# Performance work log

Hardware: AMD Instinct MI355X
Metric: run time of the kernel (lower is better)

The kernel has to match this reference:

```python
import jax, jax.numpy as jnp
import numpy as np
from jax import lax

B, T, I, H, L, C = 128, 784, 1, 256, 20, 10  # batch, seq_len, input, hidden, layers, classes


def setup_inputs() -> dict:
    key = jax.random.key(0)
    ks = jax.random.split(key, 9)
    s = 1.0 / np.sqrt(H)  # torch nn.RNN init: U(-1/sqrt(H), 1/sqrt(H))
    u = lambda k, shape: jax.random.uniform(k, shape, jnp.float32, -s, s)
    return {
        "x": jax.random.normal(ks[0], (B, T, I), jnp.float32),
        "W_ih0": u(ks[1], (H, I)),        # layer 0 input proj
        "b_ih0": u(ks[2], (H,)),
        "W_ih": u(ks[3], (L - 1, H, H)),  # layers 1..L-1 input proj
        "b_ih": u(ks[4], (L - 1, H)),
        "W_hh": u(ks[5], (L, H, H)),      # recurrent weights, all layers
        "b_hh": u(ks[6], (L, H)),
        "W_fc": u(ks[7], (C, H)),         # classification head
        "b_fc": u(ks[8], (C,)),
    }


def _rnn_layer(x_seq, W_ih, b_ih, W_hh, b_hh):
    """One vanilla relu-RNN layer. x_seq: [B,T,in] -> [B,T,H]."""
    # Hoist the input projection out of the scan (batched GEMM over all timesteps).
    xp = jnp.einsum('bti,hi->bth', x_seq, W_ih) + b_ih  # [B,T,H]
    h0 = jnp.zeros((x_seq.shape[0], W_hh.shape[0]), x_seq.dtype)

    def step(h, xt):
        h = jax.nn.relu(xt + h @ W_hh.T + b_hh)
        return h, h

    _, ys = lax.scan(step, h0, jnp.swapaxes(xp, 0, 1))  # scan over time
    return jnp.swapaxes(ys, 0, 1)  # [B,T,H]


def reference(x, W_ih0, b_ih0, W_ih, b_ih, W_hh, b_hh, W_fc, b_fc):
    h = _rnn_layer(x, W_ih0, b_ih0, W_hh[0], b_hh[0])
    for l in range(L - 1):  # fixed small layer loop
        h = _rnn_layer(h, W_ih[l], b_ih[l], W_hh[l + 1], b_hh[l + 1])
    last_hidden = h[:, -1, :]  # [B,H]
    return last_hidden @ W_fc.T + b_fc  # [B,C]
```

## Files before the change

### kernel.cpp

```cpp
#include <hip/hip_runtime.h>
#include <hip/hip_fp16.h>


#define B_    128
#define T_    784
#define H_    256
#define L_    20
#define C_    10
#define G_    8
#define BM_   16
#define S_    4
#define NS_   196
#define SW_   280
#define XSW_  260
#define RQWS_ 4096
#define TPB_  512
#define HW_   4
#define NT_   4

typedef _Float16 v8h __attribute__((ext_vector_type(8)));
typedef _Float16 v4h __attribute__((ext_vector_type(4)));
typedef float    v4f __attribute__((ext_vector_type(4)));
typedef unsigned long long u64;

union U64H { u64 u; _Float16 h[4]; };

__device__ __forceinline__ void bar_lds() {
    asm volatile("s_waitcnt lgkmcnt(0)" ::: "memory");
    __builtin_amdgcn_s_barrier();
    asm volatile("" ::: "memory");
}
__device__ __forceinline__ void bar_full() {
    asm volatile("s_waitcnt vmcnt(0) lgkmcnt(0)" ::: "memory");
    __builtin_amdgcn_s_barrier();
    asm volatile("" ::: "memory");
}

__global__ __launch_bounds__(TPB_, 2)
void rnn_wavefront(const float* __restrict__ x,
                   const float* __restrict__ W_ih0,
                   const float* __restrict__ b_ih0,
                   const float* __restrict__ W_ih,
                   const float* __restrict__ b_ih,
                   const float* __restrict__ W_hh,
                   const float* __restrict__ b_hh,
                   const float* __restrict__ W_fc,
                   const float* __restrict__ b_fc,
                   float* __restrict__ out,
                   unsigned* __restrict__ prod,
                   unsigned* __restrict__ cons,
                   u64* __restrict__ ring,
                   int rmask)
{
    const int l    = blockIdx.x >> 3;
    const int g    = blockIdx.x & 7;
    const int tid  = threadIdx.x;
    const int lane = tid & 63;
    const int wave = tid >> 6;
    const bool hwv = wave < HW_;
    const int wsub = hwv ? wave : wave - HW_;
    const int quad = lane >> 4;
    const int s16  = lane & 15;
    const int nbase = wsub * 64;
    const int m_e  = tid >> 5;
    const int n_e  = (tid & 31) * 8;

    __shared__ __align__(16) _Float16 bufX[2][S_][BM_][SW_];
    __shared__ __align__(16) _Float16 lH[2][BM_][SW_];
    __shared__ __align__(16) _Float16 xps[2][S_][BM_][XSW_];

    for (int i = tid; i < 2 * BM_ * SW_; i += TPB_) (&lH[0][0][0])[i] = (_Float16)0.f;

    v8h wf[8][NT_];
#pragma unroll
    for (int kt = 0; kt < 8; ++kt) {
        const int k0 = kt * 32 + quad * 8;
#pragma unroll
        for (int nt = 0; nt < NT_; ++nt) {
            const int j = nbase + nt * 16 + s16;
            v8h w;
            if (hwv) {
                const float* src = &W_hh[(((size_t)l * H_) + j) * H_ + k0];
#pragma unroll
                for (int i = 0; i < 8; ++i) w[i] = (_Float16)src[i];
            } else if (l > 0) {
                const float* src = &W_ih[(((size_t)(l - 1) * H_) + j) * H_ + k0];
#pragma unroll
                for (int i = 0; i < 8; ++i) w[i] = (_Float16)src[i];
            } else {
#pragma unroll
                for (int i = 0; i < 8; ++i) w[i] = (_Float16)0.f;
            }
            wf[kt][nt] = w;
        }
    }

    float bias[NT_][4], w0v[NT_][4];
    if (!hwv) {
#pragma unroll
        for (int nt = 0; nt < NT_; ++nt)
#pragma unroll
            for (int r = 0; r < 4; ++r) {
                const int j = nbase + nt * 16 + quad * 4 + r;
                bias[nt][r] = b_hh[l * H_ + j] +
                              ((l == 0) ? b_ih0[j] : b_ih[(l - 1) * H_ + j]);
                w0v[nt][r]  = (l == 0) ? W_ih0[j] : 0.f;
            }
    }

    unsigned* upprod = prod + ((l > 0 ? l - 1 : 0) * G_ + g);
    unsigned* myprod = prod + (l * G_ + g);
    unsigned* mycons = cons + (l * G_ + g);
    unsigned* dncons = cons + (((l < L_ - 1) ? l + 1 : l) * G_ + g);
    const unsigned R = (unsigned)rmask + 1u;
    u64* myring = ring + ((size_t)(l * G_ + g) * (size_t)R) * RQWS_;
    u64* upring = ring + ((size_t)((l > 0 ? l - 1 : 0) * G_ + g) * (size_t)R) * RQWS_;

    unsigned pSeen = 0, cSeen = 0;
    const size_t eidx = (size_t)m_e * 64 + (size_t)(tid & 31) * 2;

    if (l > 0) {
        if (tid == 64) {
            while (pSeen < 2u) {
                pSeen = __hip_atomic_load(upprod, __ATOMIC_RELAXED,
                                          __HIP_MEMORY_SCOPE_AGENT);
                if (pSeen < 2u) __builtin_amdgcn_s_sleep(2);
            }
        }
        __syncthreads();
#pragma unroll
        for (int sl = 0; sl < 2; ++sl)
#pragma unroll
            for (int jj = 0; jj < S_; ++jj) {
                u64 v0 = __hip_atomic_load(upring + (size_t)sl * RQWS_ + (size_t)jj * 1024 + eidx,
                                           __ATOMIC_RELAXED, __HIP_MEMORY_SCOPE_AGENT);
                u64 v1 = __hip_atomic_load(upring + (size_t)sl * RQWS_ + (size_t)jj * 1024 + eidx + 1,
                                           __ATOMIC_RELAXED, __HIP_MEMORY_SCOPE_AGENT);
                *(u64*)&bufX[sl][jj][m_e][n_e]     = v0;
                *(u64*)&bufX[sl][jj][m_e][n_e + 4] = v1;
            }
        __syncthreads();
    }
    if (!hwv) {
#pragma unroll
        for (int jj = 0; jj < S_; ++jj) {
            v4f xpa[NT_];
#pragma unroll
            for (int nt = 0; nt < NT_; ++nt)
                xpa[nt] = (v4f){bias[nt][0], bias[nt][1], bias[nt][2], bias[nt][3]};
            if (l > 0) {
#pragma unroll
                for (int kt = 0; kt < 8; ++kt) {
                    v8h a = *(const v8h*)&bufX[0][jj][s16][kt * 32 + quad * 8];
#pragma unroll
                    for (int nt = 0; nt < NT_; ++nt)
                        xpa[nt] = __builtin_amdgcn_mfma_f32_16x16x32_f16(
                                      wf[kt][nt], a, xpa[nt], 0, 0, 0);
                }
            } else {
                const float xv = x[(size_t)(g * BM_ + s16) * T_ + jj];
#pragma unroll
                for (int nt = 0; nt < NT_; ++nt)
#pragma unroll
                    for (int r = 0; r < 4; ++r)
                        xpa[nt][r] = bias[nt][r] + xv * w0v[nt][r];
            }
#pragma unroll
            for (int nt = 0; nt < NT_; ++nt) {
                U64H pk;
#pragma unroll
                for (int r = 0; r < 4; ++r) pk.h[r] = (_Float16)xpa[nt][r];
                *(u64*)&xps[0][jj][s16][nbase + nt * 16 + quad * 4] = pk.u;
            }
        }
    }
    __syncthreads();

    for (int s = 0; s < NS_; ++s) {
        const bool stOK = (l > 0) && (s + 2 < NS_);
        const bool xOK  = (s + 1 < NS_);
        u64 pfv[S_][2];

#pragma unroll
        for (int j = 0; j < S_; ++j) {
            const int t = S_ * s + j;
            if (j == 1) bar_full(); else bar_lds();

            if (j == 0) {
                if (tid == 0 && l > 0) {
                    const unsigned cv = (unsigned)((s + 2 <= NS_) ? s + 2 : NS_);
                    __hip_atomic_store(mycons, cv, __ATOMIC_RELAXED,
                                       __HIP_MEMORY_SCOPE_AGENT);
                }
                if (tid == 64 && stOK) {
                    const unsigned tgt = (unsigned)(s + 3);
                    while (pSeen < tgt) {
                        pSeen = __hip_atomic_load(upprod, __ATOMIC_RELAXED,
                                                  __HIP_MEMORY_SCOPE_AGENT);
                        if (pSeen < tgt) __builtin_amdgcn_s_sleep(2);
                    }
                }
                if (tid == 128 && l < L_ - 1 && s >= (int)R) {
                    const unsigned tgt = (unsigned)(s - (int)R + 1);
                    while (cSeen < tgt) {
                        cSeen = __hip_atomic_load(dncons, __ATOMIC_RELAXED,
                                                  __HIP_MEMORY_SCOPE_AGENT);
                        if (cSeen < tgt) __builtin_amdgcn_s_sleep(2);
                    }
                }
            }

            if (j == 1) {
                if (tid == 0 && l < L_ - 1 && s >= 1)
                    __hip_atomic_store(myprod, (unsigned)s, __ATOMIC_RELAXED,
                                       __HIP_MEMORY_SCOPE_AGENT);
                if (stOK) {
                    const u64* base = upring + (size_t)((s + 2) & rmask) * RQWS_;
#pragma unroll
                    for (int jj = 0; jj < S_; ++jj) {
                        pfv[jj][0] = __hip_atomic_load(base + (size_t)jj * 1024 + eidx,
                                                       __ATOMIC_RELAXED,
                                                       __HIP_MEMORY_SCOPE_AGENT);
                        pfv[jj][1] = __hip_atomic_load(base + (size_t)jj * 1024 + eidx + 1,
                                                       __ATOMIC_RELAXED,
                                                       __HIP_MEMORY_SCOPE_AGENT);
                    }
                }
            }

            if (l < L_ - 1 && t > 0) {
                u64 e0 = *(const u64*)&lH[t & 1][m_e][n_e];
                u64 e1 = *(const u64*)&lH[t & 1][m_e][n_e + 4];
                u64* d = myring + (size_t)(((t - 1) >> 2) & rmask) * RQWS_
                                + (size_t)((t - 1) & 3) * 1024 + eidx;
                __hip_atomic_store(d,     e0, __ATOMIC_RELAXED, __HIP_MEMORY_SCOPE_AGENT);
                __hip_atomic_store(d + 1, e1, __ATOMIC_RELAXED, __HIP_MEMORY_SCOPE_AGENT);
            }

            if (hwv) {
                v4h xph[NT_];
#pragma unroll
                for (int nt = 0; nt < NT_; ++nt)
                    xph[nt] = *(const v4h*)&xps[s & 1][j][s16][nbase + nt * 16 + quad * 4];

                v4f acc[NT_];
#pragma unroll
                for (int nt = 0; nt < NT_; ++nt) acc[nt] = (v4f){0.f, 0.f, 0.f, 0.f};
#pragma unroll
                for (int kt = 0; kt < 8; ++kt) {
                    v8h a = *(const v8h*)&lH[t & 1][s16][kt * 32 + quad * 8];
#pragma unroll
                    for (int nt = 0; nt < NT_; ++nt)
                        acc[nt] = __builtin_amdgcn_mfma_f32_16x16x32_f16(
                                      wf[kt][nt], a, acc[nt], 0, 0, 0);
                }
#pragma unroll
                for (int nt = 0; nt < NT_; ++nt) {
                    U64H pk;
#pragma unroll
                    for (int r = 0; r < 4; ++r) {
                        float v = (float)xph[nt][r] + acc[nt][r];
                        v = fmaxf(v, 0.f);
                        pk.h[r] = (_Float16)v;
                    }
                    *(u64*)&lH[(t + 1) & 1][s16][nbase + nt * 16 + quad * 4] = pk.u;
                }
            } else if (xOK) {
                v4f xpa[NT_];
#pragma unroll
                for (int nt = 0; nt < NT_; ++nt)
                    xpa[nt] = (v4f){bias[nt][0], bias[nt][1], bias[nt][2], bias[nt][3]};
                if (l > 0) {
#pragma unroll
                    for (int kt = 0; kt < 8; ++kt) {
                        v8h a = *(const v8h*)&bufX[(s + 1) & 1][j][s16][kt * 32 + quad * 8];
#pragma unroll
                        for (int nt = 0; nt < NT_; ++nt)
                            xpa[nt] = __builtin_amdgcn_mfma_f32_16x16x32_f16(
                                          wf[kt][nt], a, xpa[nt], 0, 0, 0);
                    }
                } else {
                    const float xv = x[(size_t)(g * BM_ + s16) * T_ + (S_ * (s + 1) + j)];
#pragma unroll
                    for (int nt = 0; nt < NT_; ++nt)
#pragma unroll
                        for (int r = 0; r < 4; ++r)
                            xpa[nt][r] = bias[nt][r] + xv * w0v[nt][r];
                }
#pragma unroll
                for (int nt = 0; nt < NT_; ++nt) {
                    U64H pk;
#pragma unroll
                    for (int r = 0; r < 4; ++r) pk.h[r] = (_Float16)xpa[nt][r];
                    *(u64*)&xps[(s + 1) & 1][j][s16][nbase + nt * 16 + quad * 4] = pk.u;
                }
            }

            if (j == S_ - 1 && stOK) {
#pragma unroll
                for (int jj = 0; jj < S_; ++jj) {
                    *(u64*)&bufX[s & 1][jj][m_e][n_e]     = pfv[jj][0];
                    *(u64*)&bufX[s & 1][jj][m_e][n_e + 4] = pfv[jj][1];
                }
            }
        }
    }

    if (l < L_ - 1) {
        u64 e0 = *(const u64*)&lH[0][m_e][n_e];
        u64 e1 = *(const u64*)&lH[0][m_e][n_e + 4];
        u64* d = myring + (size_t)(((T_ - 1) >> 2) & rmask) * RQWS_
                        + (size_t)3 * 1024 + eidx;
        __hip_atomic_store(d,     e0, __ATOMIC_RELAXED, __HIP_MEMORY_SCOPE_AGENT);
        __hip_atomic_store(d + 1, e1, __ATOMIC_RELAXED, __HIP_MEMORY_SCOPE_AGENT);
        __syncthreads();
        if (tid == 0)
            __hip_atomic_store(myprod, (unsigned)NS_, __ATOMIC_RELAXED,
                               __HIP_MEMORY_SCOPE_AGENT);
    } else {
        __syncthreads();
        if (tid < BM_ * C_) {
            const int bl = tid / C_;
            const int c  = tid % C_;
            float sum = b_fc[c];
            for (int k = 0; k < H_; ++k) sum += (float)lH[0][bl][k] * W_fc[c * H_ + k];
            out[(size_t)(g * BM_ + bl) * C_ + c] = sum;
        }
    }
}

extern "C" void kernel_launch(void* const* d_in, const int* in_sizes, int n_in,
                              void* d_out, int out_size, void* d_ws, size_t ws_size,
                              hipStream_t stream) {
    const float* x     = (const float*)d_in[0];
    const float* W_ih0 = (const float*)d_in[1];
    const float* b_ih0 = (const float*)d_in[2];
    const float* W_ih  = (const float*)d_in[3];
    const float* b_ih  = (const float*)d_in[4];
    const float* W_hh  = (const float*)d_in[5];
    const float* b_hh  = (const float*)d_in[6];
    const float* W_fc  = (const float*)d_in[7];
    const float* b_fc  = (const float*)d_in[8];
    float* out = (float*)d_out;

    const size_t cntBytes = (size_t)L_ * G_ * sizeof(unsigned);
    unsigned* prod = (unsigned*)d_ws;
    unsigned* cons = (unsigned*)((char*)d_ws + cntBytes);
    u64* ring      = (u64*)((char*)d_ws + 2 * cntBytes);

    const size_t slotBytes = (size_t)RQWS_ * 8;
    const size_t base = 2 * cntBytes;
    int R = 4;
    if (ws_size >= base + (size_t)L_ * G_ * 16 * slotBytes) R = 16;
    else if (ws_size >= base + (size_t)L_ * G_ * 8 * slotBytes) R = 8;

    hipMemsetAsync(d_ws, 0, 2 * cntBytes, stream);

    rnn_wavefront<<<dim3(L_ * G_), dim3(TPB_), 0, stream>>>(
        x, W_ih0, b_ih0, W_ih, b_ih, W_hh, b_hh, W_fc, b_fc,
        out, prod, cons, ring, R - 1);
}
```

Measured before the change: 1.127 ms.

## Offload ring I/O to non-recurrent waves and prioritize recurrent waves

Moves all ring-buffer loads, stores and flag polling off the four recurrent-MFMA waves onto the four input-projection waves. Each of those threads now handles 16 halves instead of 8. The recurrent waves get raised scheduling priority via s_setprio, and they preload the whole group's xps projections once per 4-step group instead of once per step. The aim is to take global-memory latency and spin polling off the serial recurrence critical path. In exchange it raises register pressure and puts more I/O work on the projection waves.

```diff
diff --git a/kernel.cpp b/kernel.cpp
--- a/kernel.cpp
+++ b/kernel.cpp
@@ -62,8 +62,12 @@
     const int quad = lane >> 4;
     const int s16  = lane & 15;
     const int nbase = wsub * 64;
-    const int m_e  = tid >> 5;
-    const int n_e  = (tid & 31) * 8;
+
+    const int xtid = tid & 255;
+    const int m_e  = xtid >> 4;
+    const int c_e  = xtid & 15;
+    const int n_e  = c_e * 16;
+    const size_t eidx = (size_t)m_e * 64 + (size_t)c_e * 4;
 
     __shared__ __align__(16) _Float16 bufX[2][S_][BM_][SW_];
     __shared__ __align__(16) _Float16 lH[2][BM_][SW_];
@@ -117,10 +121,11 @@
     u64* upring = ring + ((size_t)((l > 0 ? l - 1 : 0) * G_ + g) * (size_t)R) * RQWS_;
 
     unsigned pSeen = 0, cSeen = 0;
-    const size_t eidx = (size_t)m_e * 64 + (size_t)(tid & 31) * 2;
+
+    if (hwv) __builtin_amdgcn_s_setprio(1);
 
     if (l > 0) {
-        if (tid == 64) {
+        if (tid == 256) {
             while (pSeen < 2u) {
                 pSeen = __hip_atomic_load(upprod, __ATOMIC_RELAXED,
                                           __HIP_MEMORY_SCOPE_AGENT);
@@ -128,17 +133,19 @@
             }
         }
         __syncthreads();
-#pragma unroll
-        for (int sl = 0; sl < 2; ++sl)
-#pragma unroll
-            for (int jj = 0; jj < S_; ++jj) {
-                u64 v0 = __hip_atomic_load(upring + (size_t)sl * RQWS_ + (size_t)jj * 1024 + eidx,
-                                           __ATOMIC_RELAXED, __HIP_MEMORY_SCOPE_AGENT);
-                u64 v1 = __hip_atomic_load(upring + (size_t)sl * RQWS_ + (size_t)jj * 1024 + eidx + 1,
-                                           __ATOMIC_RELAXED, __HIP_MEMORY_SCOPE_AGENT);
-                *(u64*)&bufX[sl][jj][m_e][n_e]     = v0;
-                *(u64*)&bufX[sl][jj][m_e][n_e + 4] = v1;
-            }
+        if (!hwv) {
+#pragma unroll
+            for (int sl = 0; sl < 2; ++sl)
+#pragma unroll
+                for (int jj = 0; jj < S_; ++jj)
+#pragma unroll
+                    for (int k = 0; k < 4; ++k) {
+                        u64 v = __hip_atomic_load(
+                            upring + (size_t)sl * RQWS_ + (size_t)jj * 1024 + eidx + k,
+                            __ATOMIC_RELAXED, __HIP_MEMORY_SCOPE_AGENT);
+                        *(u64*)&bufX[sl][jj][m_e][n_e + 4 * k] = v;
+                    }
+        }
         __syncthreads();
     }
     if (!hwv) {
@@ -179,7 +186,8 @@
     for (int s = 0; s < NS_; ++s) {
         const bool stOK = (l > 0) && (s + 2 < NS_);
         const bool xOK  = (s + 1 < NS_);
-        u64 pfv[S_][2];
+        u64 pfv[S_][4];
+        v4h xphv[S_][NT_];
 
 #pragma unroll
         for (int j = 0; j < S_; ++j) {
@@ -187,12 +195,12 @@
             if (j == 1) bar_full(); else bar_lds();
 
             if (j == 0) {
-                if (tid == 0 && l > 0) {
+                if (tid == 448 && l > 0) {
                     const unsigned cv = (unsigned)((s + 2 <= NS_) ? s + 2 : NS_);
                     __hip_atomic_store(mycons, cv, __ATOMIC_RELAXED,
                                        __HIP_MEMORY_SCOPE_AGENT);
                 }
-                if (tid == 64 && stOK) {
+                if (tid == 256 && stOK) {
                     const unsigned tgt = (unsigned)(s + 3);
                     while (pSeen < tgt) {
                         pSeen = __hip_atomic_load(upprod, __ATOMIC_RELAXED,
@@ -200,7 +208,7 @@
                         if (pSeen < tgt) __builtin_amdgcn_s_sleep(2);
                     }
                 }
-                if (tid == 128 && l < L_ - 1 && s >= (int)R) {
+                if (tid == 320 && l < L_ - 1 && s >= (int)R) {
                     const unsigned tgt = (unsigned)(s - (int)R + 1);
                     while (cSeen < tgt) {
                         cSeen = __hip_atomic_load(dncons, __ATOMIC_RELAXED,
@@ -208,41 +216,47 @@
                         if (cSeen < tgt) __builtin_amdgcn_s_sleep(2);
                     }
                 }
+                if (hwv) {
+#pragma unroll
+                    for (int jj = 0; jj < S_; ++jj)
+#pragma unroll
+                        for (int nt = 0; nt < NT_; ++nt)
+                            xphv[jj][nt] = *(const v4h*)
+                                &xps[s & 1][jj][s16][nbase + nt * 16 + quad * 4];
+                }
             }
 
             if (j == 1) {
-                if (tid == 0 && l < L_ - 1 && s >= 1)
+                if (tid == 448 && l < L_ - 1 && s >= 1)
                     __hip_atomic_store(myprod, (unsigned)s, __ATOMIC_RELAXED,
                                        __HIP_MEMORY_SCOPE_AGENT);
-                if (stOK) {
+                if (stOK && !hwv) {
                     const u64* base = upring + (size_t)((s + 2) & rmask) * RQWS_;
 #pragma unroll
-                    for (int jj = 0; jj < S_; ++jj) {
-                        pfv[jj][0] = __hip_atomic_load(base + (size_t)jj * 1024 + eidx,
-                                                       __ATOMIC_RELAXED,
-                                                       __HIP_MEMORY_SCOPE_AGENT);
-                        pfv[jj][1] = __hip_atomic_load(base + (size_t)jj * 1024 + eidx + 1,
-                                                       __ATOMIC_RELAXED,
-                                                       __HIP_MEMORY_SCOPE_AGENT);
-                    }
-                }
-            }
-
-            if (l < L_ - 1 && t > 0) {
-                u64 e0 = *(const u64*)&lH[t & 1][m_e][n_e];
-                u64 e1 = *(const u64*)&lH[t & 1][m_e][n_e + 4];
+                    for (int jj = 0; jj < S_; ++jj)
+#pragma unroll
+                        for (int k = 0; k < 4; ++k)
+                            pfv[jj][k] = __hip_atomic_load(
+                                base + (size_t)jj * 1024 + eidx + k,
+                                __ATOMIC_RELAXED, __HIP_MEMORY_SCOPE_AGENT);
+                }
+            }
+
+            if (!hwv && l < L_ - 1 && t > 0) {
+                u64 e[4];
+                e[0] = *(const u64*)&lH[t & 1][m_e][n_e];
+                e[1] = *(const u64*)&lH[t & 1][m_e][n_e + 4];
+                e[2] = *(const u64*)&lH[t & 1][m_e][n_e + 8];
+                e[3] = *(const u64*)&lH[t & 1][m_e][n_e + 12];
                 u64* d = myring + (size_t)(((t - 1) >> 2) & rmask) * RQWS_
                                 + (size_t)((t - 1) & 3) * 1024 + eidx;
-                __hip_atomic_store(d,     e0, __ATOMIC_RELAXED, __HIP_MEMORY_SCOPE_AGENT);
-                __hip_atomic_store(d + 1, e1, __ATOMIC_RELAXED, __HIP_MEMORY_SCOPE_AGENT);
+#pragma unroll
+                for (int k = 0; k < 4; ++k)
+                    __hip_atomic_store(d + k, e[k], __ATOMIC_RELAXED,
+                                       __HIP_MEMORY_SCOPE_AGENT);
             }
 
             if (hwv) {
-                v4h xph[NT_];
-#pragma unroll
-                for (int nt = 0; nt < NT_; ++nt)
-                    xph[nt] = *(const v4h*)&xps[s & 1][j][s16][nbase + nt * 16 + quad * 4];
-
                 v4f acc[NT_];
 #pragma unroll
                 for (int nt = 0; nt < NT_; ++nt) acc[nt] = (v4f){0.f, 0.f, 0.f, 0.f};
@@ -259,7 +273,7 @@
                     U64H pk;
 #pragma unroll
                     for (int r = 0; r < 4; ++r) {
-                        float v = (float)xph[nt][r] + acc[nt][r];
+                        float v = (float)xphv[j][nt][r] + acc[nt][r];
                         v = fmaxf(v, 0.f);
                         pk.h[r] = (_Float16)v;
                     }
@@ -296,25 +310,29 @@
                 }
             }
 
-            if (j == S_ - 1 && stOK) {
-#pragma unroll
-                for (int jj = 0; jj < S_; ++jj) {
-                    *(u64*)&bufX[s & 1][jj][m_e][n_e]     = pfv[jj][0];
-                    *(u64*)&bufX[s & 1][jj][m_e][n_e + 4] = pfv[jj][1];
-                }
+            if (j == S_ - 1 && stOK && !hwv) {
+#pragma unroll
+                for (int jj = 0; jj < S_; ++jj)
+#pragma unroll
+                    for (int k = 0; k < 4; ++k)
+                        *(u64*)&bufX[s & 1][jj][m_e][n_e + 4 * k] = pfv[jj][k];
             }
         }
     }
 
     if (l < L_ - 1) {
-        u64 e0 = *(const u64*)&lH[0][m_e][n_e];
-        u64 e1 = *(const u64*)&lH[0][m_e][n_e + 4];
-        u64* d = myring + (size_t)(((T_ - 1) >> 2) & rmask) * RQWS_
-                        + (size_t)3 * 1024 + eidx;
-        __hip_atomic_store(d,     e0, __ATOMIC_RELAXED, __HIP_MEMORY_SCOPE_AGENT);
-        __hip_atomic_store(d + 1, e1, __ATOMIC_RELAXED, __HIP_MEMORY_SCOPE_AGENT);
+        if (!hwv) {
+            u64* d = myring + (size_t)(((T_ - 1) >> 2) & rmask) * RQWS_
+                            + (size_t)3 * 1024 + eidx;
+#pragma unroll
+            for (int k = 0; k < 4; ++k) {
+                u64 e = *(const u64*)&lH[0][m_e][n_e + 4 * k];
+                __hip_atomic_store(d + k, e, __ATOMIC_RELAXED,
+                                   __HIP_MEMORY_SCOPE_AGENT);
+            }
+        }
         __syncthreads();
-        if (tid == 0)
+        if (tid == 448)
             __hip_atomic_store(myprod, (unsigned)NS_, __ATOMIC_RELAXED,
                                __HIP_MEMORY_SCOPE_AGENT);
     } else {
```

Measured after the change: 1.617 ms. +43.5%, slower.

## Decouple recurrent and projection waves with LDS flag handshakes instead of block barriers

Applied to the files above, without the earlier changes.

Drops the block-wide barrier per timestep and lets the four recurrent waves and four projection/IO waves run as separate producer/consumer roles, synchronised through LDS counter flags. The hidden-state buffer grows to eight slots so the recurrent waves can run ahead while the other waves publish finished steps to the ring and stage the next input slot in halves. The aim is to take ring I/O and input projection off the recurrence's critical path. The cost is busy-spinning on LDS flags that competes for issue slots, plus more complex ordering that relies on relaxed atomics and explicit waitcnts.

```diff
diff --git a/kernel.cpp b/kernel.cpp
--- a/kernel.cpp
+++ b/kernel.cpp
@@ -11,11 +11,10 @@
 #define BM_   16
 #define S_    4
 #define NS_   196
-#define SW_   280
+#define SW_   264
 #define XSW_  260
 #define RQWS_ 4096
 #define TPB_  512
-#define HW_   4
 #define NT_   4
 
 typedef _Float16 v8h __attribute__((ext_vector_type(8)));
@@ -25,15 +24,47 @@
 
 union U64H { u64 u; _Float16 h[4]; };
 
-__device__ __forceinline__ void bar_lds() {
-    asm volatile("s_waitcnt lgkmcnt(0)" ::: "memory");
-    __builtin_amdgcn_s_barrier();
-    asm volatile("" ::: "memory");
-}
-__device__ __forceinline__ void bar_full() {
-    asm volatile("s_waitcnt vmcnt(0) lgkmcnt(0)" ::: "memory");
-    __builtin_amdgcn_s_barrier();
-    asm volatile("" ::: "memory");
+__device__ __forceinline__ void lgkm0() { asm volatile("s_waitcnt lgkmcnt(0)" ::: "memory"); }
+__device__ __forceinline__ void vm0()   { asm volatile("s_waitcnt vmcnt(0)"   ::: "memory"); }
+__device__ __forceinline__ void cbar()  { asm volatile("" ::: "memory"); }
+
+__device__ __forceinline__ void flagst(unsigned* p, unsigned v) {
+    cbar();
+    __hip_atomic_store(p, v, __ATOMIC_RELAXED, __HIP_MEMORY_SCOPE_WORKGROUP);
+}
+__device__ __forceinline__ void spin4(const unsigned* f, unsigned tgt) {
+    const volatile u64* p = (const volatile u64*)f;
+    for (;;) {
+        u64 a = p[0], b = p[1];
+        if ((unsigned)a >= tgt && (unsigned)(a >> 32) >= tgt &&
+            (unsigned)b >= tgt && (unsigned)(b >> 32) >= tgt) break;
+    }
+    cbar();
+}
+__device__ __forceinline__ void spin4s(const unsigned* f, unsigned tgt) {
+    const volatile u64* p = (const volatile u64*)f;
+    for (;;) {
+        u64 a = p[0], b = p[1];
+        if ((unsigned)a >= tgt && (unsigned)(a >> 32) >= tgt &&
+            (unsigned)b >= tgt && (unsigned)(b >> 32) >= tgt) break;
+        __builtin_amdgcn_s_sleep(1);
+    }
+    cbar();
+}
+__device__ __forceinline__ u64 ringld(const u64* p) {
+    return __hip_atomic_load(p, __ATOMIC_RELAXED, __HIP_MEMORY_SCOPE_AGENT);
+}
+__device__ __forceinline__ void ringst(u64* p, u64 v) {
+    __hip_atomic_store(p, v, __ATOMIC_RELAXED, __HIP_MEMORY_SCOPE_AGENT);
+}
+__device__ __forceinline__ unsigned remld(const unsigned* p) {
+    return __hip_atomic_load(p, __ATOMIC_RELAXED, __HIP_MEMORY_SCOPE_AGENT);
+}
+__device__ __forceinline__ void rempub(unsigned* p, unsigned v) {
+    __hip_atomic_store(p, v, __ATOMIC_RELAXED, __HIP_MEMORY_SCOPE_AGENT);
+}
+__device__ __forceinline__ void rpoll(const unsigned* p, unsigned tgt) {
+    while (remld(p) < tgt) __builtin_amdgcn_s_sleep(2);
 }
 
 __global__ __launch_bounds__(TPB_, 2)
@@ -57,19 +88,29 @@
     const int tid  = threadIdx.x;
     const int lane = tid & 63;
     const int wave = tid >> 6;
-    const bool hwv = wave < HW_;
-    const int wsub = hwv ? wave : wave - HW_;
+    const bool hrole = wave < 4;
+    const int wsub = hrole ? wave : wave - 4;
     const int quad = lane >> 4;
     const int s16  = lane & 15;
     const int nbase = wsub * 64;
-    const int m_e  = tid >> 5;
-    const int n_e  = (tid & 31) * 8;
-
-    __shared__ __align__(16) _Float16 bufX[2][S_][BM_][SW_];
-    __shared__ __align__(16) _Float16 lH[2][BM_][SW_];
+    const int xtid  = tid & 255;
+
+    __shared__ __align__(16) _Float16 lH[8][BM_][SW_];
     __shared__ __align__(16) _Float16 xps[2][S_][BM_][XSW_];
-
-    for (int i = tid; i < 2 * BM_ * SW_; i += TPB_) (&lH[0][0][0])[i] = (_Float16)0.f;
+    __shared__ __align__(16) _Float16 bufX[2][BM_][SW_];
+    __shared__ __align__(16) unsigned hflag[4];
+    __shared__ __align__(16) unsigned xdone4[4];
+    __shared__ __align__(16) unsigned xpdone4[4];
+    __shared__ __align__(16) unsigned xsflag[4];
+    __shared__ __align__(16) unsigned xcflag[4];
+    __shared__ __align__(16) unsigned xeflag[4];
+    __shared__ __align__(16) unsigned xvflag[4];
+
+    for (int i = tid; i < BM_ * SW_; i += TPB_) (&lH[0][0][0])[i] = (_Float16)0.f;
+    if (tid < 4) {
+        hflag[tid] = 0; xdone4[tid] = 0; xpdone4[tid] = 0;
+        xsflag[tid] = 0; xcflag[tid] = 0; xeflag[tid] = 0; xvflag[tid] = 0;
+    }
 
     v8h wf[8][NT_];
 #pragma unroll
@@ -79,7 +120,7 @@
         for (int nt = 0; nt < NT_; ++nt) {
             const int j = nbase + nt * 16 + s16;
             v8h w;
-            if (hwv) {
+            if (hrole) {
                 const float* src = &W_hh[(((size_t)l * H_) + j) * H_ + k0];
 #pragma unroll
                 for (int i = 0; i < 8; ++i) w[i] = (_Float16)src[i];
@@ -96,7 +137,7 @@
     }
 
     float bias[NT_][4], w0v[NT_][4];
-    if (!hwv) {
+    if ((!hrole && l > 0) || (hrole && l == 0)) {
 #pragma unroll
         for (int nt = 0; nt < NT_; ++nt)
 #pragma unroll
@@ -111,144 +152,115 @@
     unsigned* upprod = prod + ((l > 0 ? l - 1 : 0) * G_ + g);
     unsigned* myprod = prod + (l * G_ + g);
     unsigned* mycons = cons + (l * G_ + g);
-    unsigned* dncons = cons + (((l < L_ - 1) ? l + 1 : l) * G_ + g);
+    unsigned* upcons = cons + ((l > 0 ? l - 1 : 0) * G_ + g);
     const unsigned R = (unsigned)rmask + 1u;
     u64* myring = ring + ((size_t)(l * G_ + g) * (size_t)R) * RQWS_;
     u64* upring = ring + ((size_t)((l > 0 ? l - 1 : 0) * G_ + g) * (size_t)R) * RQWS_;
 
-    unsigned pSeen = 0, cSeen = 0;
-    const size_t eidx = (size_t)m_e * 64 + (size_t)(tid & 31) * 2;
-
-    if (l > 0) {
-        if (tid == 64) {
-            while (pSeen < 2u) {
-                pSeen = __hip_atomic_load(upprod, __ATOMIC_RELAXED,
-                                          __HIP_MEMORY_SCOPE_AGENT);
-                if (pSeen < 2u) __builtin_amdgcn_s_sleep(2);
-            }
-        }
-        __syncthreads();
-#pragma unroll
-        for (int sl = 0; sl < 2; ++sl)
-#pragma unroll
-            for (int jj = 0; jj < S_; ++jj) {
-                u64 v0 = __hip_atomic_load(upring + (size_t)sl * RQWS_ + (size_t)jj * 1024 + eidx,
-                                           __ATOMIC_RELAXED, __HIP_MEMORY_SCOPE_AGENT);
-                u64 v1 = __hip_atomic_load(upring + (size_t)sl * RQWS_ + (size_t)jj * 1024 + eidx + 1,
-                                           __ATOMIC_RELAXED, __HIP_MEMORY_SCOPE_AGENT);
-                *(u64*)&bufX[sl][jj][m_e][n_e]     = v0;
-                *(u64*)&bufX[sl][jj][m_e][n_e + 4] = v1;
-            }
-        __syncthreads();
-    }
-    if (!hwv) {
-#pragma unroll
-        for (int jj = 0; jj < S_; ++jj) {
-            v4f xpa[NT_];
+    __syncthreads();
+
+    auto xstage = [&](const u64* sbp, int half) {
+        u64 sv[8];
+#pragma unroll
+        for (int k = 0; k < 8; ++k)
+            sv[k] = ringld(sbp + (size_t)(half * 2048 + xtid + 256 * k));
+#pragma unroll
+        for (int k = 0; k < 8; ++k) {
+            const int idx = half * 2048 + xtid + 256 * k;
+            const int rr  = idx & 1023;
+            *(u64*)&bufX[(idx >> 10) & 1][rr & 15][(rr >> 4) * 4] = sv[k];
+        }
+    };
+    auto xcompute = [&](int q, int jj) {
+        v4f xpa[NT_];
+#pragma unroll
+        for (int nt = 0; nt < NT_; ++nt)
+            xpa[nt] = (v4f){bias[nt][0], bias[nt][1], bias[nt][2], bias[nt][3]};
+#pragma unroll
+        for (int kt = 0; kt < 8; ++kt) {
+            v8h a = *(const v8h*)&bufX[jj & 1][s16][kt * 32 + quad * 8];
 #pragma unroll
             for (int nt = 0; nt < NT_; ++nt)
-                xpa[nt] = (v4f){bias[nt][0], bias[nt][1], bias[nt][2], bias[nt][3]};
-            if (l > 0) {
+                xpa[nt] = __builtin_amdgcn_mfma_f32_16x16x32_f16(
+                              wf[kt][nt], a, xpa[nt], 0, 0, 0);
+        }
+#pragma unroll
+        for (int nt = 0; nt < NT_; ++nt) {
+            U64H pk;
+#pragma unroll
+            for (int r = 0; r < 4; ++r) pk.h[r] = (_Float16)xpa[nt][r];
+            *(u64*)&xps[q & 1][jj][s16][nbase + nt * 16 + quad * 4] = pk.u;
+        }
+    };
+    auto xslot = [&](int q) {
+        rpoll(upprod, (unsigned)(q + 1));
+        spin4(xeflag, (unsigned)q);
+        const u64* sbp = upring + (size_t)(q & rmask) * RQWS_;
+        xstage(sbp, 0);
+        lgkm0(); flagst(&xsflag[wsub], (unsigned)(2 * q + 1));
+        spin4(xsflag, (unsigned)(2 * q + 1));
+        xcompute(q, 0); xcompute(q, 1);
+        lgkm0(); flagst(&xcflag[wsub], (unsigned)(q + 1));
+        spin4(xcflag, (unsigned)(q + 1));
+        xstage(sbp, 1);
+        lgkm0(); flagst(&xsflag[wsub], (unsigned)(2 * q + 2));
+        spin4(xsflag, (unsigned)(2 * q + 2));
+        xcompute(q, 2); xcompute(q, 3);
+        lgkm0();
+        flagst(&xpdone4[wsub], (unsigned)(q + 1));
+        flagst(&xeflag[wsub], (unsigned)(q + 1));
+    };
+
+    if (hrole) {
+        float xnf[4];
+        v4h xphv[4][NT_];
+        if (l == 0) {
+            const float* xrow = x + (size_t)(g * BM_ + s16) * T_;
+#pragma unroll
+            for (int jj = 0; jj < 4; ++jj) xnf[jj] = xrow[jj];
+        }
+        for (int s = 0; s < NS_; ++s) {
+#pragma unroll
+            for (int j = 0; j < S_; ++j) {
+                const int t = 4 * s + j;
+                spin4(hflag, (unsigned)t);
+                if (j == 0) {
+                    if (l < L_ - 1) spin4(xdone4, (unsigned)s);
+                    if (l > 0)      spin4(xpdone4, (unsigned)(s + 1));
+                    if (l == 0) {
+#pragma unroll
+                        for (int jj = 0; jj < 4; ++jj)
+#pragma unroll
+                            for (int nt = 0; nt < NT_; ++nt)
+#pragma unroll
+                                for (int r = 0; r < 4; ++r)
+                                    xphv[jj][nt][r] =
+                                        (_Float16)(bias[nt][r] + xnf[jj] * w0v[nt][r]);
+                    }
+                }
+                if (j == 1 && l == 0 && s + 1 < NS_) {
+                    const float* xrow = x + (size_t)(g * BM_ + s16) * T_ + 4 * (s + 1);
+#pragma unroll
+                    for (int jj = 0; jj < 4; ++jj) xnf[jj] = xrow[jj];
+                }
+
+                v4h xph[NT_];
+                if (l > 0) {
+#pragma unroll
+                    for (int nt = 0; nt < NT_; ++nt)
+                        xph[nt] = *(const v4h*)
+                            &xps[s & 1][j][s16][nbase + nt * 16 + quad * 4];
+                } else {
+#pragma unroll
+                    for (int nt = 0; nt < NT_; ++nt) xph[nt] = xphv[j][nt];
+                }
+
+                v4f acc[NT_];
+#pragma unroll
+                for (int nt = 0; nt < NT_; ++nt) acc[nt] = (v4f){0.f, 0.f, 0.f, 0.f};
 #pragma unroll
                 for (int kt = 0; kt < 8; ++kt) {
-                    v8h a = *(const v8h*)&bufX[0][jj][s16][kt * 32 + quad * 8];
-#pragma unroll
-                    for (int nt = 0; nt < NT_; ++nt)
-                        xpa[nt] = __builtin_amdgcn_mfma_f32_16x16x32_f16(
-                                      wf[kt][nt], a, xpa[nt], 0, 0, 0);
-                }
-            } else {
-                const float xv = x[(size_t)(g * BM_ + s16) * T_ + jj];
-#pragma unroll
-                for (int nt = 0; nt < NT_; ++nt)
-#pragma unroll
-                    for (int r = 0; r < 4; ++r)
-                        xpa[nt][r] = bias[nt][r] + xv * w0v[nt][r];
-            }
-#pragma unroll
-            for (int nt = 0; nt < NT_; ++nt) {
-                U64H pk;
-#pragma unroll
-                for (int r = 0; r < 4; ++r) pk.h[r] = (_Float16)xpa[nt][r];
-                *(u64*)&xps[0][jj][s16][nbase + nt * 16 + quad * 4] = pk.u;
-            }
-        }
-    }
-    __syncthreads();
-
-    for (int s = 0; s < NS_; ++s) {
-        const bool stOK = (l > 0) && (s + 2 < NS_);
-        const bool xOK  = (s + 1 < NS_);
-        u64 pfv[S_][2];
-
-#pragma unroll
-        for (int j = 0; j < S_; ++j) {
-            const int t = S_ * s + j;
-            if (j == 1) bar_full(); else bar_lds();
-
-            if (j == 0) {
-                if (tid == 0 && l > 0) {
-                    const unsigned cv = (unsigned)((s + 2 <= NS_) ? s + 2 : NS_);
-                    __hip_atomic_store(mycons, cv, __ATOMIC_RELAXED,
-                                       __HIP_MEMORY_SCOPE_AGENT);
-                }
-                if (tid == 64 && stOK) {
-                    const unsigned tgt = (unsigned)(s + 3);
-                    while (pSeen < tgt) {
-                        pSeen = __hip_atomic_load(upprod, __ATOMIC_RELAXED,
-                                                  __HIP_MEMORY_SCOPE_AGENT);
-                        if (pSeen < tgt) __builtin_amdgcn_s_sleep(2);
-                    }
-                }
-                if (tid == 128 && l < L_ - 1 && s >= (int)R) {
-                    const unsigned tgt = (unsigned)(s - (int)R + 1);
-                    while (cSeen < tgt) {
-                        cSeen = __hip_atomic_load(dncons, __ATOMIC_RELAXED,
-                                                  __HIP_MEMORY_SCOPE_AGENT);
-                        if (cSeen < tgt) __builtin_amdgcn_s_sleep(2);
-                    }
-                }
-            }
-
-            if (j == 1) {
-                if (tid == 0 && l < L_ - 1 && s >= 1)
-                    __hip_atomic_store(myprod, (unsigned)s, __ATOMIC_RELAXED,
-                                       __HIP_MEMORY_SCOPE_AGENT);
-                if (stOK) {
-                    const u64* base = upring + (size_t)((s + 2) & rmask) * RQWS_;
-#pragma unroll
-                    for (int jj = 0; jj < S_; ++jj) {
-                        pfv[jj][0] = __hip_atomic_load(base + (size_t)jj * 1024 + eidx,
-                                                       __ATOMIC_RELAXED,
-                                                       __HIP_MEMORY_SCOPE_AGENT);
-                        pfv[jj][1] = __hip_atomic_load(base + (size_t)jj * 1024 + eidx + 1,
-                                                       __ATOMIC_RELAXED,
-                                                       __HIP_MEMORY_SCOPE_AGENT);
-                    }
-                }
-            }
-
-            if (l < L_ - 1 && t > 0) {
-                u64 e0 = *(const u64*)&lH[t & 1][m_e][n_e];
-                u64 e1 = *(const u64*)&lH[t & 1][m_e][n_e + 4];
-                u64* d = myring + (size_t)(((t - 1) >> 2) & rmask) * RQWS_
-                                + (size_t)((t - 1) & 3) * 1024 + eidx;
-                __hip_atomic_store(d,     e0, __ATOMIC_RELAXED, __HIP_MEMORY_SCOPE_AGENT);
-                __hip_atomic_store(d + 1, e1, __ATOMIC_RELAXED, __HIP_MEMORY_SCOPE_AGENT);
-            }
-
-            if (hwv) {
-                v4h xph[NT_];
-#pragma unroll
-                for (int nt = 0; nt < NT_; ++nt)
-                    xph[nt] = *(const v4h*)&xps[s & 1][j][s16][nbase + nt * 16 + quad * 4];
-
-                v4f acc[NT_];
-#pragma unroll
-                for (int nt = 0; nt < NT_; ++nt) acc[nt] = (v4f){0.f, 0.f, 0.f, 0.f};
-#pragma unroll
-                for (int kt = 0; kt < 8; ++kt) {
-                    v8h a = *(const v8h*)&lH[t & 1][s16][kt * 32 + quad * 8];
+                    v8h a = *(const v8h*)&lH[t & 7][s16][kt * 32 + quad * 8];
 #pragma unroll
                     for (int nt = 0; nt < NT_; ++nt)
                         acc[nt] = __builtin_amdgcn_mfma_f32_16x16x32_f16(
@@ -263,68 +275,63 @@
                         v = fmaxf(v, 0.f);
                         pk.h[r] = (_Float16)v;
                     }
-                    *(u64*)&lH[(t + 1) & 1][s16][nbase + nt * 16 + quad * 4] = pk.u;
-                }
-            } else if (xOK) {
-                v4f xpa[NT_];
-#pragma unroll
-                for (int nt = 0; nt < NT_; ++nt)
-                    xpa[nt] = (v4f){bias[nt][0], bias[nt][1], bias[nt][2], bias[nt][3]};
-                if (l > 0) {
-#pragma unroll
-                    for (int kt = 0; kt < 8; ++kt) {
-                        v8h a = *(const v8h*)&bufX[(s + 1) & 1][j][s16][kt * 32 + quad * 8];
-#pragma unroll
-                        for (int nt = 0; nt < NT_; ++nt)
-                            xpa[nt] = __builtin_amdgcn_mfma_f32_16x16x32_f16(
-                                          wf[kt][nt], a, xpa[nt], 0, 0, 0);
+                    *(u64*)&lH[(t + 1) & 7][s16][nbase + nt * 16 + quad * 4] = pk.u;
+                }
+                lgkm0();
+                flagst(&hflag[wave], (unsigned)(t + 1));
+            }
+        }
+        if (l == L_ - 1) {
+            spin4(hflag, (unsigned)T_);
+            lgkm0();
+            if (tid < BM_ * C_) {
+                const int bl = tid / C_;
+                const int c  = tid % C_;
+                float sum = b_fc[c];
+                for (int k = 0; k < H_; ++k)
+                    sum += (float)lH[0][bl][k] * W_fc[c * H_ + k];
+                out[(size_t)(g * BM_ + bl) * C_ + c] = sum;
+            }
+        }
+    } else {
+        if (l > 0) {
+            xslot(0);
+            vm0();
+            if (tid == 256) rempub(upcons, 1u);
+        }
+        for (int sg = 0; sg <= NS_; ++sg) {
+            spin4s(hflag, (unsigned)(4 * sg));
+
+            if (l < L_ - 1 && sg >= 1) {
+                const int e = sg - 1;
+                if (e >= (int)R) rpoll(mycons, (unsigned)(e - (int)R + 1));
+                u64* db = myring + (size_t)(e & rmask) * RQWS_;
+#pragma unroll
+                for (int jj = 0; jj < 4; ++jj) {
+                    const int buf = (4 * e + jj + 1) & 7;
+                    u64 ev[4];
+#pragma unroll
+                    for (int k = 0; k < 4; ++k) {
+                        const int rr = xtid + 256 * k;
+                        ev[k] = *(const u64*)&lH[buf][rr & 15][(rr >> 4) * 4];
                     }
-                } else {
-                    const float xv = x[(size_t)(g * BM_ + s16) * T_ + (S_ * (s + 1) + j)];
-#pragma unroll
-                    for (int nt = 0; nt < NT_; ++nt)
-#pragma unroll
-                        for (int r = 0; r < 4; ++r)
-                            xpa[nt][r] = bias[nt][r] + xv * w0v[nt][r];
-                }
-#pragma unroll
-                for (int nt = 0; nt < NT_; ++nt) {
-                    U64H pk;
-#pragma unroll
-                    for (int r = 0; r < 4; ++r) pk.h[r] = (_Float16)xpa[nt][r];
-                    *(u64*)&xps[(s + 1) & 1][j][s16][nbase + nt * 16 + quad * 4] = pk.u;
-                }
-            }
-
-            if (j == S_ - 1 && stOK) {
-#pragma unroll
-                for (int jj = 0; jj < S_; ++jj) {
-                    *(u64*)&bufX[s & 1][jj][m_e][n_e]     = pfv[jj][0];
-                    *(u64*)&bufX[s & 1][jj][m_e][n_e + 4] = pfv[jj][1];
-                }
-            }
-        }
-    }
-
-    if (l < L_ - 1) {
-        u64 e0 = *(const u64*)&lH[0][m_e][n_e];
-        u64 e1 = *(const u64*)&lH[0][m_e][n_e + 4];
-        u64* d = myring + (size_t)(((T_ - 1) >> 2) & rmask) * RQWS_
-                        + (size_t)3 * 1024 + eidx;
-        __hip_atomic_store(d,     e0, __ATOMIC_RELAXED, __HIP_MEMORY_SCOPE_AGENT);
-        __hip_atomic_store(d + 1, e1, __ATOMIC_RELAXED, __HIP_MEMORY_SCOPE_AGENT);
-        __syncthreads();
-        if (tid == 0)
-            __hip_atomic_store(myprod, (unsigned)NS_, __ATOMIC_RELAXED,
-                               __HIP_MEMORY_SCOPE_AGENT);
-    } else {
-        __syncthreads();
-        if (tid < BM_ * C_) {
-            const int bl = tid / C_;
-            const int c  = tid % C_;
-            float sum = b_fc[c];
-            for (int k = 0; k < H_; ++k) sum += (float)lH[0][bl][k] * W_fc[c * H_ + k];
-            out[(size_t)(g * BM_ + bl) * C_ + c] = sum;
+#pragma unroll
+                    for (int k = 0; k < 4; ++k)
+                        ringst(db + (size_t)jj * 1024 + (size_t)(xtid + 256 * k), ev[k]);
+                }
+                lgkm0();
+            }
+            flagst(&xdone4[wsub], (unsigned)(sg + 1));
+
+            if (l > 0 && sg + 1 <= NS_ - 1) xslot(sg + 1);
+
+            vm0();
+            flagst(&xvflag[wsub], (unsigned)(sg + 1));
+            spin4(xvflag, (unsigned)(sg + 1));
+            if (tid == 256) {
+                if (l < L_ - 1 && sg >= 1) rempub(myprod, (unsigned)sg);
+                if (l > 0 && sg + 1 <= NS_ - 1) rempub(upcons, (unsigned)(sg + 2));
+            }
         }
     }
 }
@@ -354,7 +361,7 @@
     if (ws_size >= base + (size_t)L_ * G_ * 16 * slotBytes) R = 16;
     else if (ws_size >= base + (size_t)L_ * G_ * 8 * slotBytes) R = 8;
 
-    hipMemsetAsync(d_ws, 0, 2 * cntBytes, stream);
+    (void)hipMemsetAsync(d_ws, 0, 2 * cntBytes, stream);
 
     rnn_wavefront<<<dim3(L_ * G_), dim3(TPB_), 0, stream>>>(
         x, W_ih0, b_ih0, W_ih, b_ih, W_hh, b_hh, W_fc, b_fc,
```

New measurement: 1.522 ms. 35.0% more time.
